# Optimization experiments

Hardware: AMD Instinct MI355X
Metric: run time of the kernel (lower is better)

Reference implementation:

```python
import jax, jax.numpy as jnp
import numpy as np

N_NODES = 50000
N_EDGES = 800000
IN_DIM, HID_DIM, OUT_DIM = 1024, 256, 512


def setup_inputs() -> dict:
    key = jax.random.key(0)
    ks = jax.random.split(key, 8)
    x = jax.random.normal(ks[0], (N_NODES, IN_DIM), dtype=jnp.float32)
    edge_index = jax.random.randint(ks[1], (2, N_EDGES), 0, N_NODES, dtype=jnp.int64)
    # Glorot-ish scaled weights; PyG SAGEConv: out = lin_l(mean_aggr) + lin_r(x), bias in lin_l
    w1_l = jax.random.normal(ks[2], (HID_DIM, IN_DIM), dtype=jnp.float32) / np.sqrt(IN_DIM)
    w1_r = jax.random.normal(ks[3], (HID_DIM, IN_DIM), dtype=jnp.float32) / np.sqrt(IN_DIM)
    b1 = jnp.zeros((HID_DIM,), dtype=jnp.float32)
    w2_l = jax.random.normal(ks[4], (OUT_DIM, HID_DIM), dtype=jnp.float32) / np.sqrt(HID_DIM)
    w2_r = jax.random.normal(ks[5], (OUT_DIM, HID_DIM), dtype=jnp.float32) / np.sqrt(HID_DIM)
    b2 = jnp.zeros((OUT_DIM,), dtype=jnp.float32)
    return {"x": x, "edge_index": edge_index, "w1_l": w1_l, "w1_r": w1_r, "b1": b1,
            "w2_l": w2_l, "w2_r": w2_r, "b2": b2}


def _sage_conv(x, edge_index, w_l, w_r, b):
    """PyG SAGEConv with mean aggregation: lin_l(mean_{j in N(i)} x_j) + lin_r(x_i)."""
    src, dst = edge_index[0], edge_index[1]
    n = x.shape[0]
    # gather source features and scatter-mean into destinations (the memory-bound part)
    agg = jax.ops.segment_sum(x[src], dst, num_segments=n)          # [N, d_in]
    cnt = jax.ops.segment_sum(jnp.ones_like(src, dtype=x.dtype), dst, num_segments=n)
    mean = agg / jnp.maximum(cnt, 1.0)[:, None]                     # empty neighborhoods -> 0
    return mean @ w_l.T + x @ w_r.T + b


def reference(x, edge_index, w1_l, w1_r, b1, w2_l, w2_r, b2):
    # layer 1 + relu (dropout is identity in eval mode)
    h = jax.nn.relu(_sage_conv(x, edge_index, w1_l, w1_r, b1))
    # final layer, no activation
    return _sage_conv(h, edge_index, w2_l, w2_r, b2)
```

## Files before the change

### kernel.cpp

```cpp
#include <hip/hip_runtime.h>


#define IN_DIM  1024
#define HID_DIM 256
#define OUT_N   512

typedef __attribute__((ext_vector_type(8))) short bf16x8;
typedef __attribute__((ext_vector_type(4))) float f32x4;

static __device__ __forceinline__ unsigned short f2bf(float f) {
  unsigned int u = __float_as_uint(f);
  u += 0x7fffu + ((u >> 16) & 1u);
  return (unsigned short)(u >> 16);
}
static __device__ __forceinline__ float bf2f(unsigned short b) {
  return __uint_as_float(((unsigned int)b) << 16);
}

static __device__ __forceinline__ int load_idx(const void* ei, long long pos, int is64) {
  if (is64) return (int)((const long long*)ei)[pos];
  return ((const int*)ei)[pos];
}

__global__ void k_misc(const unsigned int* __restrict__ ei, int* __restrict__ flag,
                       const float* __restrict__ w1l, const float* __restrict__ w1r,
                       unsigned short* __restrict__ W1c,
                       const float* __restrict__ w2l, const float* __restrict__ w2r,
                       unsigned short* __restrict__ W2c) {
  int b = blockIdx.x;
  if (b == 0) {
    if (threadIdx.x < 64) {
      unsigned int v = ei[2 * threadIdx.x + 1];
      unsigned long long m = __ballot(v == 0u);
      if (threadIdx.x == 0) *flag = (m == ~0ull) ? 1 : 0;
    }
    return;
  }
  b -= 1;
  if (b < 512) {
    int i = b * 256 + threadIdx.x;
    int base = i * 4;
    int n = base / IN_DIM, k = base % IN_DIM;
    const float* s = (n < HID_DIM) ? &w1l[(size_t)n * IN_DIM + k]
                                   : &w1r[(size_t)(n - HID_DIM) * IN_DIM + k];
    float4 v = *(const float4*)s;
    ushort4 o = { f2bf(v.x), f2bf(v.y), f2bf(v.z), f2bf(v.w) };
    *(ushort4*)&W1c[base] = o;
  } else {
    int i = (b - 512) * 256 + threadIdx.x;
    int base = i * 4;
    int n = base >> 9, k = base & 511;
    const float* s = (k < HID_DIM) ? &w2l[(size_t)n * HID_DIM + k]
                                   : &w2r[(size_t)n * HID_DIM + (k - HID_DIM)];
    float4 v = *(const float4*)s;
    ushort4 o = { f2bf(v.x), f2bf(v.y), f2bf(v.z), f2bf(v.w) };
    *(ushort4*)&W2c[base] = o;
  }
}

__global__ void k_cvt_x(const float* __restrict__ x, unsigned short* __restrict__ xbf, int n4) {
  int i = blockIdx.x * 256 + threadIdx.x;
  if (i >= n4) return;
  float4 v = ((const float4*)x)[i];
  ushort4 o = { f2bf(v.x), f2bf(v.y), f2bf(v.z), f2bf(v.w) };
  ((ushort4*)xbf)[i] = o;
}

__global__ void k_deg(const void* ei, int nE, const int* flag, int* deg) {
  int e = blockIdx.x * 256 + threadIdx.x;
  if (e >= nE) return;
  int d = load_idx(ei, (long long)nE + e, *flag);
  atomicAdd(&deg[d], 1);
}

__global__ __launch_bounds__(1024) void k_scan(const int* __restrict__ deg,
                                               int* __restrict__ off, int n) {
  __shared__ int sums[1024];
  int t = threadIdx.x;
  int chunk = (n + 1023) >> 10;
  int base = t * chunk;
  int s = 0;
  for (int i = 0; i < chunk; ++i) { int idx = base + i; if (idx < n) s += deg[idx]; }
  sums[t] = s;
  __syncthreads();
  for (int d = 1; d < 1024; d <<= 1) {
    int v = 0;
    if (t >= d) v = sums[t - d];
    __syncthreads();
    sums[t] += v;
    __syncthreads();
  }
  int run = (t == 0) ? 0 : sums[t - 1];
  for (int i = 0; i < chunk; ++i) {
    int idx = base + i;
    if (idx < n) { off[idx] = run; run += deg[idx]; }
  }
  if (t == 1023) off[n] = run;
}

__global__ void k_fill(const void* ei, int nE, const int* flag,
                       const int* __restrict__ off, int* cursor, int* __restrict__ csr) {
  int e = blockIdx.x * 256 + threadIdx.x;
  if (e >= nE) return;
  int is64 = *flag;
  int s = load_idx(ei, e, is64);
  int d = load_idx(ei, (long long)nE + e, is64);
  int p = atomicAdd(&cursor[d], 1);
  csr[off[d] + p] = s;
}

static __device__ __forceinline__ void load_lds16(const void* g, void* lds) {
  __builtin_amdgcn_global_load_lds(
      (const __attribute__((address_space(1))) unsigned int*)g,
      (__attribute__((address_space(3))) unsigned int*)lds, 16, 0, 0);
}

__global__ __launch_bounds__(256) void k_gemm1(const unsigned short* __restrict__ A,
                                               const unsigned short* __restrict__ B,
                                               unsigned short* __restrict__ Cl,
                                               unsigned short* __restrict__ Cr,
                                               const float* __restrict__ b1) {
  __shared__ unsigned short As[128 * 32];
  __shared__ unsigned short Bs[128 * 32];
  const int tid = threadIdx.x;
  const int w = tid >> 6, l = tid & 63;
  const int wm = w >> 1, wn = w & 1;
  const int quad = l >> 4, lane16 = l & 15;
  const int m0 = blockIdx.y * 128;
  const int n0 = blockIdx.x * 128;

  f32x4 acc[4][4] = {};
  for (int k0 = 0; k0 < IN_DIM; k0 += 32) {
#pragma unroll
    for (int c = 0; c < 2; ++c) {
      const int flat = ((w * 2 + c) << 10);
      const int fb = flat + l * 16;
      const int row = fb >> 6;
      const int cb = fb & 63;
      load_lds16(A + (size_t)(m0 + row) * IN_DIM + (k0 + (cb >> 1)), (char*)As + flat);
      load_lds16(B + (size_t)(n0 + row) * IN_DIM + (k0 + (cb >> 1)), (char*)Bs + flat);
    }
    __syncthreads();
    bf16x8 af[4], bfr[4];
#pragma unroll
    for (int i = 0; i < 4; ++i)
      af[i] = *(const bf16x8*)&As[(wm * 64 + i * 16 + lane16) * 32 + quad * 8];
#pragma unroll
    for (int j = 0; j < 4; ++j)
      bfr[j] = *(const bf16x8*)&Bs[(wn * 64 + j * 16 + lane16) * 32 + quad * 8];
#pragma unroll
    for (int i = 0; i < 4; ++i)
#pragma unroll
      for (int j = 0; j < 4; ++j)
        acc[i][j] = __builtin_amdgcn_mfma_f32_16x16x32_bf16(af[i], bfr[j], acc[i][j], 0, 0, 0);
    __syncthreads();
  }

  const bool right = (n0 >= 256);
  unsigned short* Cb = right ? Cr : Cl;
  const int nc0 = n0 - (right ? 256 : 0);
#pragma unroll
  for (int i = 0; i < 4; ++i) {
    const int rbase = m0 + wm * 64 + i * 16 + quad * 4;
#pragma unroll
    for (int j = 0; j < 4; ++j) {
      const int col = nc0 + wn * 64 + j * 16 + lane16;
      const float bv = right ? b1[col] : 0.0f;
#pragma unroll
      for (int r = 0; r < 4; ++r)
        Cb[(size_t)(rbase + r) * HID_DIM + col] = f2bf(acc[i][j][r] + bv);
    }
  }
}

__global__ __launch_bounds__(256) void k_gemm2(const unsigned short* __restrict__ Am,
                                               const unsigned short* __restrict__ Ah,
                                               const unsigned short* __restrict__ B,
                                               float* __restrict__ out,
                                               const float* __restrict__ b2, int Mstore) {
  __shared__ unsigned short As[128 * 32];
  __shared__ unsigned short Bs[128 * 32];
  const int tid = threadIdx.x;
  const int w = tid >> 6, l = tid & 63;
  const int wm = w >> 1, wn = w & 1;
  const int quad = l >> 4, lane16 = l & 15;
  const int m0 = blockIdx.y * 128;
  const int n0 = blockIdx.x * 128;

  f32x4 acc[4][4] = {};
  for (int k0 = 0; k0 < 2 * HID_DIM; k0 += 32) {
    const unsigned short* Abase = (k0 < HID_DIM) ? Am + k0 : Ah + (k0 - HID_DIM);
#pragma unroll
    for (int c = 0; c < 2; ++c) {
      const int flat = ((w * 2 + c) << 10);
      const int fb = flat + l * 16;
      const int row = fb >> 6;
      const int cb = fb & 63;
      load_lds16(Abase + (size_t)(m0 + row) * HID_DIM + (cb >> 1), (char*)As + flat);
      load_lds16(B + (size_t)(n0 + row) * (2 * HID_DIM) + (k0 + (cb >> 1)), (char*)Bs + flat);
    }
    __syncthreads();
    bf16x8 af[4], bfr[4];
#pragma unroll
    for (int i = 0; i < 4; ++i)
      af[i] = *(const bf16x8*)&As[(wm * 64 + i * 16 + lane16) * 32 + quad * 8];
#pragma unroll
    for (int j = 0; j < 4; ++j)
      bfr[j] = *(const bf16x8*)&Bs[(wn * 64 + j * 16 + lane16) * 32 + quad * 8];
#pragma unroll
    for (int i = 0; i < 4; ++i)
#pragma unroll
      for (int j = 0; j < 4; ++j)
        acc[i][j] = __builtin_amdgcn_mfma_f32_16x16x32_bf16(af[i], bfr[j], acc[i][j], 0, 0, 0);
    __syncthreads();
  }

#pragma unroll
  for (int i = 0; i < 4; ++i) {
    const int rbase = m0 + wm * 64 + i * 16 + quad * 4;
#pragma unroll
    for (int j = 0; j < 4; ++j) {
      const int col = n0 + wn * 64 + j * 16 + lane16;
      const float bv = b2[col];
#pragma unroll
      for (int r = 0; r < 4; ++r) {
        const int rowi = rbase + r;
        if (rowi < Mstore) out[(size_t)rowi * OUT_N + col] = acc[i][j][r] + bv;
      }
    }
  }
}

__global__ void k_agg1(const unsigned short* __restrict__ Cl,
                       const unsigned short* __restrict__ Cr,
                       const int* __restrict__ off, const int* __restrict__ csr,
                       unsigned short* __restrict__ h, int nNodes) {
  int node = blockIdx.x * 4 + (threadIdx.x >> 6);
  int l = threadIdx.x & 63;
  if (node >= nNodes) return;
  int s = off[node], e = off[node + 1];
  float a0 = 0.f, a1 = 0.f, a2 = 0.f, a3 = 0.f;
  int i = s;
  for (; i + 4 <= e; i += 4) {
    int s0 = csr[i], s1 = csr[i + 1], s2 = csr[i + 2], s3 = csr[i + 3];
    ushort4 v0 = *(const ushort4*)&Cl[(size_t)s0 * HID_DIM + l * 4];
    ushort4 v1 = *(const ushort4*)&Cl[(size_t)s1 * HID_DIM + l * 4];
    ushort4 v2 = *(const ushort4*)&Cl[(size_t)s2 * HID_DIM + l * 4];
    ushort4 v3 = *(const ushort4*)&Cl[(size_t)s3 * HID_DIM + l * 4];
    a0 += bf2f(v0.x) + bf2f(v1.x) + bf2f(v2.x) + bf2f(v3.x);
    a1 += bf2f(v0.y) + bf2f(v1.y) + bf2f(v2.y) + bf2f(v3.y);
    a2 += bf2f(v0.z) + bf2f(v1.z) + bf2f(v2.z) + bf2f(v3.z);
    a3 += bf2f(v0.w) + bf2f(v1.w) + bf2f(v2.w) + bf2f(v3.w);
  }
  for (; i < e; ++i) {
    int s0 = csr[i];
    ushort4 v = *(const ushort4*)&Cl[(size_t)s0 * HID_DIM + l * 4];
    a0 += bf2f(v.x); a1 += bf2f(v.y); a2 += bf2f(v.z); a3 += bf2f(v.w);
  }
  float inv = 1.0f / fmaxf((float)(e - s), 1.0f);
  ushort4 xr = *(const ushort4*)&Cr[(size_t)node * HID_DIM + l * 4];
  ushort4 o = { f2bf(fmaxf(a0 * inv + bf2f(xr.x), 0.0f)),
                f2bf(fmaxf(a1 * inv + bf2f(xr.y), 0.0f)),
                f2bf(fmaxf(a2 * inv + bf2f(xr.z), 0.0f)),
                f2bf(fmaxf(a3 * inv + bf2f(xr.w), 0.0f)) };
  *(ushort4*)&h[(size_t)node * HID_DIM + l * 4] = o;
}

__global__ void k_agg2(const unsigned short* __restrict__ h,
                       const int* __restrict__ off, const int* __restrict__ csr,
                       unsigned short* __restrict__ mean2, int nNodes) {
  int node = blockIdx.x * 4 + (threadIdx.x >> 6);
  int l = threadIdx.x & 63;
  if (node >= nNodes) return;
  int s = off[node], e = off[node + 1];
  float a0 = 0.f, a1 = 0.f, a2 = 0.f, a3 = 0.f;
  int i = s;
  for (; i + 4 <= e; i += 4) {
    int s0 = csr[i], s1 = csr[i + 1], s2 = csr[i + 2], s3 = csr[i + 3];
    ushort4 v0 = *(const ushort4*)&h[(size_t)s0 * HID_DIM + l * 4];
    ushort4 v1 = *(const ushort4*)&h[(size_t)s1 * HID_DIM + l * 4];
    ushort4 v2 = *(const ushort4*)&h[(size_t)s2 * HID_DIM + l * 4];
    ushort4 v3 = *(const ushort4*)&h[(size_t)s3 * HID_DIM + l * 4];
    a0 += bf2f(v0.x) + bf2f(v1.x) + bf2f(v2.x) + bf2f(v3.x);
    a1 += bf2f(v0.y) + bf2f(v1.y) + bf2f(v2.y) + bf2f(v3.y);
    a2 += bf2f(v0.z) + bf2f(v1.z) + bf2f(v2.z) + bf2f(v3.z);
    a3 += bf2f(v0.w) + bf2f(v1.w) + bf2f(v2.w) + bf2f(v3.w);
  }
  for (; i < e; ++i) {
    int s0 = csr[i];
    ushort4 v = *(const ushort4*)&h[(size_t)s0 * HID_DIM + l * 4];
    a0 += bf2f(v.x); a1 += bf2f(v.y); a2 += bf2f(v.z); a3 += bf2f(v.w);
  }
  float inv = 1.0f / fmaxf((float)(e - s), 1.0f);
  ushort4 o = { f2bf(a0 * inv), f2bf(a1 * inv), f2bf(a2 * inv), f2bf(a3 * inv) };
  *(ushort4*)&mean2[(size_t)node * HID_DIM + l * 4] = o;
}

extern "C" void kernel_launch(void* const* d_in, const int* in_sizes, int n_in,
                              void* d_out, int out_size, void* d_ws, size_t ws_size,
                              hipStream_t stream) {
  const float* x   = (const float*)d_in[0];
  const void*  ei  = d_in[1];
  const float* w1l = (const float*)d_in[2];
  const float* w1r = (const float*)d_in[3];
  const float* b1  = (const float*)d_in[4];
  const float* w2l = (const float*)d_in[5];
  const float* w2r = (const float*)d_in[6];
  const float* b2  = (const float*)d_in[7];
  float* out = (float*)d_out;

  const int nN   = in_sizes[0] / IN_DIM;
  const int nE   = in_sizes[1] / 2;
  const int Mpad = (nN + 127) & ~127;

  char* ws = (char*)d_ws;
  size_t o = 0;
  auto alloc = [&](size_t bytes) {
    char* p = ws + o;
    o += (bytes + 255) & ~(size_t)255;
    return p;
  };
  unsigned short* xbf   = (unsigned short*)alloc((size_t)Mpad * IN_DIM * 2);
  unsigned short* W1c   = (unsigned short*)alloc((size_t)2 * HID_DIM * IN_DIM * 2);
  unsigned short* W2c   = (unsigned short*)alloc((size_t)OUT_N * 2 * HID_DIM * 2);
  unsigned short* Cl    = (unsigned short*)alloc((size_t)Mpad * HID_DIM * 2);
  unsigned short* Cr    = (unsigned short*)alloc((size_t)Mpad * HID_DIM * 2);
  unsigned short* hbuf  = (unsigned short*)alloc((size_t)Mpad * HID_DIM * 2);
  unsigned short* mean2 = (unsigned short*)alloc((size_t)Mpad * HID_DIM * 2);
  int* deg    = (int*)alloc((size_t)nN * 4);
  int* offs   = (int*)alloc((size_t)(nN + 1) * 4);
  int* cursor = (int*)alloc((size_t)nN * 4);
  int* csr    = (int*)alloc((size_t)nE * 4);
  int* flag   = (int*)alloc(256);

  hipMemsetAsync(deg, 0, (size_t)nN * 4, stream);
  hipMemsetAsync(cursor, 0, (size_t)nN * 4, stream);

  k_misc<<<1 + 512 + 256, 256, 0, stream>>>((const unsigned int*)ei, flag,
                                            w1l, w1r, W1c, w2l, w2r, W2c);
  k_cvt_x<<<(nN * IN_DIM / 4 + 255) / 256, 256, 0, stream>>>(x, xbf, nN * IN_DIM / 4);
  k_deg<<<(nE + 255) / 256, 256, 0, stream>>>(ei, nE, flag, deg);
  k_scan<<<1, 1024, 0, stream>>>(deg, offs, nN);
  k_fill<<<(nE + 255) / 256, 256, 0, stream>>>(ei, nE, flag, offs, cursor, csr);

  dim3 g1(512 / 128, Mpad / 128);
  k_gemm1<<<g1, 256, 0, stream>>>(xbf, W1c, Cl, Cr, b1);
  k_agg1<<<(nN + 3) / 4, 256, 0, stream>>>(Cl, Cr, offs, csr, hbuf, nN);
  k_agg2<<<(nN + 3) / 4, 256, 0, stream>>>(hbuf, offs, csr, mean2, nN);
  k_gemm2<<<g1, 256, 0, stream>>>(mean2, hbuf, W2c, out, b2, nN);
}
```

Measured before the change: 753.8 us.

## Vectorize aggregation gathers, stage GEMM1 epilogue through LDS, fold degree count into misc

The aggregation kernels now load 16-byte bf16x8 rows, with each half-wavefront handling alternate neighbors, and combine the halves with a cross-lane shuffle. This widens the gather loads and doubles the edges in flight per wave. The GEMM1 epilogue stages accumulators in LDS so each thread writes 16 contiguous bf16 values with vector stores instead of scattered 2-byte writes. The degree-count kernel and the index-width flag are folded into the weight-conversion kernel, with each thread re-detecting the width, which removes one launch at the cost of an extra LDS round trip and more barriers in the epilogue.

```diff
diff --git a/kernel.cpp b/kernel.cpp
--- a/kernel.cpp
+++ b/kernel.cpp
@@ -6,6 +6,7 @@
 #define OUT_N   512
 
 typedef __attribute__((ext_vector_type(8))) short bf16x8;
+typedef __attribute__((ext_vector_type(8))) unsigned short u16x8;
 typedef __attribute__((ext_vector_type(4))) float f32x4;
 
 static __device__ __forceinline__ unsigned short f2bf(float f) {
@@ -17,44 +18,43 @@
   return __uint_as_float(((unsigned int)b) << 16);
 }
 
+static __device__ __forceinline__ int detect64(const void* ei) {
+  const unsigned int* p = (const unsigned int*)ei;
+  return (p[1] | p[3] | p[5] | p[7]) == 0u;
+}
 static __device__ __forceinline__ int load_idx(const void* ei, long long pos, int is64) {
   if (is64) return (int)((const long long*)ei)[pos];
   return ((const int*)ei)[pos];
 }
 
-__global__ void k_misc(const unsigned int* __restrict__ ei, int* __restrict__ flag,
+__global__ void k_misc(const void* __restrict__ ei, int nE,
                        const float* __restrict__ w1l, const float* __restrict__ w1r,
                        unsigned short* __restrict__ W1c,
                        const float* __restrict__ w2l, const float* __restrict__ w2r,
-                       unsigned short* __restrict__ W2c) {
+                       unsigned short* __restrict__ W2c, int* __restrict__ deg) {
   int b = blockIdx.x;
-  if (b == 0) {
-    if (threadIdx.x < 64) {
-      unsigned int v = ei[2 * threadIdx.x + 1];
-      unsigned long long m = __ballot(v == 0u);
-      if (threadIdx.x == 0) *flag = (m == ~0ull) ? 1 : 0;
-    }
-    return;
-  }
-  b -= 1;
   if (b < 512) {
-    int i = b * 256 + threadIdx.x;
-    int base = i * 4;
+    int base = (b * 256 + threadIdx.x) * 4;
     int n = base / IN_DIM, k = base % IN_DIM;
     const float* s = (n < HID_DIM) ? &w1l[(size_t)n * IN_DIM + k]
                                    : &w1r[(size_t)(n - HID_DIM) * IN_DIM + k];
     float4 v = *(const float4*)s;
     ushort4 o = { f2bf(v.x), f2bf(v.y), f2bf(v.z), f2bf(v.w) };
     *(ushort4*)&W1c[base] = o;
-  } else {
-    int i = (b - 512) * 256 + threadIdx.x;
-    int base = i * 4;
+  } else if (b < 768) {
+    int base = ((b - 512) * 256 + threadIdx.x) * 4;
     int n = base >> 9, k = base & 511;
     const float* s = (k < HID_DIM) ? &w2l[(size_t)n * HID_DIM + k]
                                    : &w2r[(size_t)n * HID_DIM + (k - HID_DIM)];
     float4 v = *(const float4*)s;
     ushort4 o = { f2bf(v.x), f2bf(v.y), f2bf(v.z), f2bf(v.w) };
     *(ushort4*)&W2c[base] = o;
+  } else {
+    int e = (b - 768) * 256 + threadIdx.x;
+    if (e >= nE) return;
+    int is64 = detect64(ei);
+    int d = load_idx(ei, (long long)nE + e, is64);
+    atomicAdd(&deg[d], 1);
   }
 }
 
@@ -64,13 +64,6 @@
   float4 v = ((const float4*)x)[i];
   ushort4 o = { f2bf(v.x), f2bf(v.y), f2bf(v.z), f2bf(v.w) };
   ((ushort4*)xbf)[i] = o;
-}
-
-__global__ void k_deg(const void* ei, int nE, const int* flag, int* deg) {
-  int e = blockIdx.x * 256 + threadIdx.x;
-  if (e >= nE) return;
-  int d = load_idx(ei, (long long)nE + e, *flag);
-  atomicAdd(&deg[d], 1);
 }
 
 __global__ __launch_bounds__(1024) void k_scan(const int* __restrict__ deg,
@@ -98,11 +91,11 @@
   if (t == 1023) off[n] = run;
 }
 
-__global__ void k_fill(const void* ei, int nE, const int* flag,
+__global__ void k_fill(const void* __restrict__ ei, int nE,
                        const int* __restrict__ off, int* cursor, int* __restrict__ csr) {
   int e = blockIdx.x * 256 + threadIdx.x;
   if (e >= nE) return;
-  int is64 = *flag;
+  int is64 = detect64(ei);
   int s = load_idx(ei, e, is64);
   int d = load_idx(ei, (long long)nE + e, is64);
   int p = atomicAdd(&cursor[d], 1);
@@ -114,14 +107,17 @@
       (const __attribute__((address_space(1))) unsigned int*)g,
       (__attribute__((address_space(3))) unsigned int*)lds, 16, 0, 0);
 }
+
+#define LSTRIDE 132
 
 __global__ __launch_bounds__(256) void k_gemm1(const unsigned short* __restrict__ A,
                                                const unsigned short* __restrict__ B,
                                                unsigned short* __restrict__ Cl,
                                                unsigned short* __restrict__ Cr,
                                                const float* __restrict__ b1) {
-  __shared__ unsigned short As[128 * 32];
-  __shared__ unsigned short Bs[128 * 32];
+  __shared__ char SMEM[32 * LSTRIDE * 4];
+  unsigned short* As = (unsigned short*)SMEM;
+  unsigned short* Bs = As + 128 * 32;
   const int tid = threadIdx.x;
   const int w = tid >> 6, l = tid & 63;
   const int wm = w >> 1, wn = w & 1;
@@ -159,17 +155,40 @@
   const bool right = (n0 >= 256);
   unsigned short* Cb = right ? Cr : Cl;
   const int nc0 = n0 - (right ? 256 : 0);
+  const int rrow = tid >> 3;
+  const int rcol = (tid & 7) * 16;
+  float bias_r[16];
+#pragma unroll
+  for (int k = 0; k < 4; ++k) {
+    if (right) *(float4*)&bias_r[k * 4] = *(const float4*)&b1[nc0 + rcol + k * 4];
+    else { bias_r[k*4] = 0.f; bias_r[k*4+1] = 0.f; bias_r[k*4+2] = 0.f; bias_r[k*4+3] = 0.f; }
+  }
+  float* Ls = (float*)SMEM;
 #pragma unroll
   for (int i = 0; i < 4; ++i) {
-    const int rbase = m0 + wm * 64 + i * 16 + quad * 4;
+    __syncthreads();
+    const int lr = wm * 16 + quad * 4;
 #pragma unroll
     for (int j = 0; j < 4; ++j) {
-      const int col = nc0 + wn * 64 + j * 16 + lane16;
-      const float bv = right ? b1[col] : 0.0f;
+      const int lc = wn * 64 + j * 16 + lane16;
 #pragma unroll
       for (int r = 0; r < 4; ++r)
-        Cb[(size_t)(rbase + r) * HID_DIM + col] = f2bf(acc[i][j][r] + bv);
-    }
+        Ls[(lr + r) * LSTRIDE + lc] = acc[i][j][r];
+    }
+    __syncthreads();
+    float v[16];
+#pragma unroll
+    for (int k = 0; k < 4; ++k)
+      *(float4*)&v[k * 4] = *(const float4*)&Ls[rrow * LSTRIDE + rcol + k * 4];
+    u16x8 o0, o1;
+#pragma unroll
+    for (int k = 0; k < 8; ++k) {
+      o0[k] = (short)f2bf(v[k] + bias_r[k]);
+      o1[k] = (short)f2bf(v[k + 8] + bias_r[k + 8]);
+    }
+    const int grow = m0 + (rrow >> 4) * 64 + i * 16 + (rrow & 15);
+    *(u16x8*)&Cb[(size_t)grow * HID_DIM + nc0 + rcol] = o0;
+    *(u16x8*)&Cb[(size_t)grow * HID_DIM + nc0 + rcol + 8] = o1;
   }
 }
 
@@ -236,64 +255,88 @@
                        const int* __restrict__ off, const int* __restrict__ csr,
                        unsigned short* __restrict__ h, int nNodes) {
   int node = blockIdx.x * 4 + (threadIdx.x >> 6);
+  if (node >= nNodes) return;
   int l = threadIdx.x & 63;
-  if (node >= nNodes) return;
+  int half = l >> 5, lc = l & 31;
   int s = off[node], e = off[node + 1];
-  float a0 = 0.f, a1 = 0.f, a2 = 0.f, a3 = 0.f;
+  float acc[8] = {};
   int i = s;
-  for (; i + 4 <= e; i += 4) {
-    int s0 = csr[i], s1 = csr[i + 1], s2 = csr[i + 2], s3 = csr[i + 3];
-    ushort4 v0 = *(const ushort4*)&Cl[(size_t)s0 * HID_DIM + l * 4];
-    ushort4 v1 = *(const ushort4*)&Cl[(size_t)s1 * HID_DIM + l * 4];
-    ushort4 v2 = *(const ushort4*)&Cl[(size_t)s2 * HID_DIM + l * 4];
-    ushort4 v3 = *(const ushort4*)&Cl[(size_t)s3 * HID_DIM + l * 4];
-    a0 += bf2f(v0.x) + bf2f(v1.x) + bf2f(v2.x) + bf2f(v3.x);
-    a1 += bf2f(v0.y) + bf2f(v1.y) + bf2f(v2.y) + bf2f(v3.y);
-    a2 += bf2f(v0.z) + bf2f(v1.z) + bf2f(v2.z) + bf2f(v3.z);
-    a3 += bf2f(v0.w) + bf2f(v1.w) + bf2f(v2.w) + bf2f(v3.w);
-  }
-  for (; i < e; ++i) {
-    int s0 = csr[i];
-    ushort4 v = *(const ushort4*)&Cl[(size_t)s0 * HID_DIM + l * 4];
-    a0 += bf2f(v.x); a1 += bf2f(v.y); a2 += bf2f(v.z); a3 += bf2f(v.w);
-  }
-  float inv = 1.0f / fmaxf((float)(e - s), 1.0f);
-  ushort4 xr = *(const ushort4*)&Cr[(size_t)node * HID_DIM + l * 4];
-  ushort4 o = { f2bf(fmaxf(a0 * inv + bf2f(xr.x), 0.0f)),
-                f2bf(fmaxf(a1 * inv + bf2f(xr.y), 0.0f)),
-                f2bf(fmaxf(a2 * inv + bf2f(xr.z), 0.0f)),
-                f2bf(fmaxf(a3 * inv + bf2f(xr.w), 0.0f)) };
-  *(ushort4*)&h[(size_t)node * HID_DIM + l * 4] = o;
+  for (; i + 8 <= e; i += 8) {
+    int r0 = csr[i + half], r1 = csr[i + 2 + half], r2 = csr[i + 4 + half], r3 = csr[i + 6 + half];
+    u16x8 v0 = *(const u16x8*)&Cl[(size_t)r0 * HID_DIM + lc * 8];
+    u16x8 v1 = *(const u16x8*)&Cl[(size_t)r1 * HID_DIM + lc * 8];
+    u16x8 v2 = *(const u16x8*)&Cl[(size_t)r2 * HID_DIM + lc * 8];
+    u16x8 v3 = *(const u16x8*)&Cl[(size_t)r3 * HID_DIM + lc * 8];
+#pragma unroll
+    for (int k = 0; k < 8; ++k)
+      acc[k] += (bf2f(v0[k]) + bf2f(v1[k])) + (bf2f(v2[k]) + bf2f(v3[k]));
+  }
+  for (; i + 2 <= e; i += 2) {
+    int r0 = csr[i + half];
+    u16x8 v0 = *(const u16x8*)&Cl[(size_t)r0 * HID_DIM + lc * 8];
+#pragma unroll
+    for (int k = 0; k < 8; ++k) acc[k] += bf2f(v0[k]);
+  }
+  if (i < e && half == 0) {
+    int r0 = csr[i];
+    u16x8 v0 = *(const u16x8*)&Cl[(size_t)r0 * HID_DIM + lc * 8];
+#pragma unroll
+    for (int k = 0; k < 8; ++k) acc[k] += bf2f(v0[k]);
+  }
+#pragma unroll
+  for (int k = 0; k < 8; ++k) acc[k] += __shfl_xor(acc[k], 32);
+  if (half == 0) {
+    float inv = 1.0f / fmaxf((float)(e - s), 1.0f);
+    u16x8 xr = *(const u16x8*)&Cr[(size_t)node * HID_DIM + lc * 8];
+    u16x8 o;
+#pragma unroll
+    for (int k = 0; k < 8; ++k)
+      o[k] = (short)f2bf(fmaxf(acc[k] * inv + bf2f(xr[k]), 0.0f));
+    *(u16x8*)&h[(size_t)node * HID_DIM + lc * 8] = o;
+  }
 }
 
 __global__ void k_agg2(const unsigned short* __restrict__ h,
                        const int* __restrict__ off, const int* __restrict__ csr,
                        unsigned short* __restrict__ mean2, int nNodes) {
   int node = blockIdx.x * 4 + (threadIdx.x >> 6);
+  if (node >= nNodes) return;
   int l = threadIdx.x & 63;
-  if (node >= nNodes) return;
+  int half = l >> 5, lc = l & 31;
   int s = off[node], e = off[node + 1];
-  float a0 = 0.f, a1 = 0.f, a2 = 0.f, a3 = 0.f;
+  float acc[8] = {};
   int i = s;
-  for (; i + 4 <= e; i += 4) {
-    int s0 = csr[i], s1 = csr[i + 1], s2 = csr[i + 2], s3 = csr[i + 3];
-    ushort4 v0 = *(const ushort4*)&h[(size_t)s0 * HID_DIM + l * 4];
-    ushort4 v1 = *(const ushort4*)&h[(size_t)s1 * HID_DIM + l * 4];
-    ushort4 v2 = *(const ushort4*)&h[(size_t)s2 * HID_DIM + l * 4];
-    ushort4 v3 = *(const ushort4*)&h[(size_t)s3 * HID_DIM + l * 4];
-    a0 += bf2f(v0.x) + bf2f(v1.x) + bf2f(v2.x) + bf2f(v3.x);
-    a1 += bf2f(v0.y) + bf2f(v1.y) + bf2f(v2.y) + bf2f(v3.y);
-    a2 += bf2f(v0.z) + bf2f(v1.z) + bf2f(v2.z) + bf2f(v3.z);
-    a3 += bf2f(v0.w) + bf2f(v1.w) + bf2f(v2.w) + bf2f(v3.w);
-  }
-  for (; i < e; ++i) {
-    int s0 = csr[i];
-    ushort4 v = *(const ushort4*)&h[(size_t)s0 * HID_DIM + l * 4];
-    a0 += bf2f(v.x); a1 += bf2f(v.y); a2 += bf2f(v.z); a3 += bf2f(v.w);
-  }
-  float inv = 1.0f / fmaxf((float)(e - s), 1.0f);
-  ushort4 o = { f2bf(a0 * inv), f2bf(a1 * inv), f2bf(a2 * inv), f2bf(a3 * inv) };
-  *(ushort4*)&mean2[(size_t)node * HID_DIM + l * 4] = o;
+  for (; i + 8 <= e; i += 8) {
+    int r0 = csr[i + half], r1 = csr[i + 2 + half], r2 = csr[i + 4 + half], r3 = csr[i + 6 + half];
+    u16x8 v0 = *(const u16x8*)&h[(size_t)r0 * HID_DIM + lc * 8];
+    u16x8 v1 = *(const u16x8*)&h[(size_t)r1 * HID_DIM + lc * 8];
+    u16x8 v2 = *(const u16x8*)&h[(size_t)r2 * HID_DIM + lc * 8];
+    u16x8 v3 = *(const u16x8*)&h[(size_t)r3 * HID_DIM + lc * 8];
+#pragma unroll
+    for (int k = 0; k < 8; ++k)
+      acc[k] += (bf2f(v0[k]) + bf2f(v1[k])) + (bf2f(v2[k]) + bf2f(v3[k]));
+  }
+  for (; i + 2 <= e; i += 2) {
+    int r0 = csr[i + half];
+    u16x8 v0 = *(const u16x8*)&h[(size_t)r0 * HID_DIM + lc * 8];
+#pragma unroll
+    for (int k = 0; k < 8; ++k) acc[k] += bf2f(v0[k]);
+  }
+  if (i < e && half == 0) {
+    int r0 = csr[i];
+    u16x8 v0 = *(const u16x8*)&h[(size_t)r0 * HID_DIM + lc * 8];
+#pragma unroll
+    for (int k = 0; k < 8; ++k) acc[k] += bf2f(v0[k]);
+  }
+#pragma unroll
+  for (int k = 0; k < 8; ++k) acc[k] += __shfl_xor(acc[k], 32);
+  if (half == 0) {
+    float inv = 1.0f / fmaxf((float)(e - s), 1.0f);
+    u16x8 o;
+#pragma unroll
+    for (int k = 0; k < 8; ++k) o[k] = (short)f2bf(acc[k] * inv);
+    *(u16x8*)&mean2[(size_t)node * HID_DIM + lc * 8] = o;
+  }
 }
 
 extern "C" void kernel_launch(void* const* d_in, const int* in_sizes, int n_in,
@@ -331,17 +374,15 @@
   int* offs   = (int*)alloc((size_t)(nN + 1) * 4);
   int* cursor = (int*)alloc((size_t)nN * 4);
   int* csr    = (int*)alloc((size_t)nE * 4);
-  int* flag   = (int*)alloc(256);
 
   hipMemsetAsync(deg, 0, (size_t)nN * 4, stream);
   hipMemsetAsync(cursor, 0, (size_t)nN * 4, stream);
 
-  k_misc<<<1 + 512 + 256, 256, 0, stream>>>((const unsigned int*)ei, flag,
-                                            w1l, w1r, W1c, w2l, w2r, W2c);
+  const int degBlocks = (nE + 255) / 256;
+  k_misc<<<768 + degBlocks, 256, 0, stream>>>(ei, nE, w1l, w1r, W1c, w2l, w2r, W2c, deg);
   k_cvt_x<<<(nN * IN_DIM / 4 + 255) / 256, 256, 0, stream>>>(x, xbf, nN * IN_DIM / 4);
-  k_deg<<<(nE + 255) / 256, 256, 0, stream>>>(ei, nE, flag, deg);
   k_scan<<<1, 1024, 0, stream>>>(deg, offs, nN);
-  k_fill<<<(nE + 255) / 256, 256, 0, stream>>>(ei, nE, flag, offs, cursor, csr);
+  k_fill<<<(nE + 255) / 256, 256, 0, stream>>>(ei, nE, offs, cursor, csr);
 
   dim3 g1(512 / 128, Mpad / 128);
   k_gemm1<<<g1, 256, 0, stream>>>(xbf, W1c, Cl, Cr, b1);
```

Measured after the change: 766.8 us. About the same (+1.7%).
